# Kernel tuning notes

Hardware: AMD Instinct MI355X
Metric: run time of the kernel (lower is better)

The kernel has to match this reference:

```python
import jax, jax.numpy as jnp
import numpy as np

N = 8192
F_IN = 128
F_OUT = 128
NEG_SLOPE = 0.2


def setup_inputs() -> dict:
    key = jax.random.key(0)
    k_h, k_adj, k_W, k_a = jax.random.split(key, 4)
    h = jax.random.normal(k_h, (N, F_IN), dtype=jnp.float32)
    # binary adjacency mask as float (the module multiplies scores by adj)
    adj = (jax.random.uniform(k_adj, (N, N)) < 0.05).astype(jnp.float32)
    # nn.Linear(in, out, bias=False): weight shape [out, in]
    W = jax.random.normal(k_W, (F_OUT, F_IN), dtype=jnp.float32) / np.sqrt(F_IN)
    # nn.Linear(2*out, 1, bias=False): weight shape [1, 2*out]
    a = jax.random.normal(k_a, (1, 2 * F_OUT), dtype=jnp.float32) / np.sqrt(2 * F_OUT)
    return {"h": h, "adj": adj, "W": W, "a": a}


def reference(h, adj, W, a):
    # Wh: [N, F_out]
    Wh = h @ W.T
    f = Wh.shape[-1]
    # a([Wh_i ; Wh_j]) factored: e[i, j] = leaky_relu(Wh[i]@a1 + Wh[j]@a2)
    a1 = a[0, :f]  # [F_out]
    a2 = a[0, f:]  # [F_out]
    s_i = Wh @ a1  # [N]
    s_j = Wh @ a2  # [N]
    e = jax.nn.leaky_relu(s_i[:, None] + s_j[None, :], NEG_SLOPE)  # [N, N]
    # faithful to original: softmax over dim=1 of e * adj (multiplicative mask)
    attention = jax.nn.softmax(e * adj, axis=1)  # [N, N]
    return attention @ Wh  # [N, F_out]
```

## Files before the change

kernel.cpp:

```cpp
#include <hip/hip_runtime.h>

#define N_NODES 8192
#define FDIM 128
#define NEG_SLOPE 0.2f
#define SEG 512

__global__ __launch_bounds__(256) void wh_fused_kernel(
    const float* __restrict__ h, const float* __restrict__ W,
    float* __restrict__ Wh, float* __restrict__ S) {
  __shared__ float Wt[FDIM * 132];
  __shared__ float rows[32 * 132];
  const int t = threadIdx.x;
  const int base = blockIdx.x * 32;
  for (int it = 0; it < 64; ++it) {
    int idx = t + 256 * it;
    int o = idx >> 7, k = idx & 127;
    Wt[k * 132 + o] = W[idx];
  }
  for (int it = 0; it < 16; ++it) {
    int idx = t + 256 * it;
    int r = idx >> 7, col = idx & 127;
    rows[r * 132 + col] = h[(size_t)base * FDIM + idx];
  }
  __syncthreads();
  const int c4 = (t & 31) * 4;
  const int g = t >> 5;
  float acc[4][4];
#pragma unroll
  for (int rr = 0; rr < 4; ++rr)
#pragma unroll
    for (int cc = 0; cc < 4; ++cc) acc[rr][cc] = 0.f;
  for (int k = 0; k < FDIM; ++k) {
    float4 wv = *(const float4*)&Wt[k * 132 + c4];
    float rv[4];
#pragma unroll
    for (int rr = 0; rr < 4; ++rr) rv[rr] = rows[(4 * g + rr) * 132 + k];
#pragma unroll
    for (int rr = 0; rr < 4; ++rr) {
      acc[rr][0] += rv[rr] * wv.x;
      acc[rr][1] += rv[rr] * wv.y;
      acc[rr][2] += rv[rr] * wv.z;
      acc[rr][3] += rv[rr] * wv.w;
    }
  }
#pragma unroll
  for (int rr = 0; rr < 4; ++rr) {
    int r = base + 4 * g + rr;
    *(float4*)&Wh[(size_t)r * FDIM + c4] =
        make_float4(acc[rr][0], acc[rr][1], acc[rr][2], acc[rr][3]);
  }
  __syncthreads();
  float4 cs = make_float4(acc[0][0] + acc[1][0] + acc[2][0] + acc[3][0],
                          acc[0][1] + acc[1][1] + acc[2][1] + acc[3][1],
                          acc[0][2] + acc[1][2] + acc[2][2] + acc[3][2],
                          acc[0][3] + acc[1][3] + acc[2][3] + acc[3][3]);
  *(float4*)&rows[g * FDIM + c4] = cs;
  __syncthreads();
  if (t < FDIM) {
    float s = 0.f;
#pragma unroll
    for (int gg = 0; gg < 8; ++gg) s += rows[gg * FDIM + t];
    atomicAdd(&S[t], s);
  }
}

__global__ __launch_bounds__(256) void scores_kernel(
    const float* __restrict__ Wh, const float* __restrict__ a,
    float* __restrict__ s1, float* __restrict__ s2) {
  const int t = threadIdx.x;
  const int lane = t & 63;
  const int wave = t >> 6;
  const int row = blockIdx.x * 4 + wave;
  float v0 = Wh[(size_t)row * FDIM + lane];
  float v1 = Wh[(size_t)row * FDIM + 64 + lane];
  float d1 = v0 * a[lane] + v1 * a[64 + lane];
  float d2 = v0 * a[FDIM + lane] + v1 * a[FDIM + 64 + lane];
  for (int off = 32; off; off >>= 1) {
    d1 += __shfl_down(d1, off);
    d2 += __shfl_down(d2, off);
  }
  if (lane == 0) { s1[row] = d1; s2[row] = d2; }
}

__device__ __forceinline__ float4 ntload4(const float4* p) {
  typedef float f4v __attribute__((ext_vector_type(4)));
  f4v v = __builtin_nontemporal_load((const f4v*)p);
  return make_float4(v[0], v[1], v[2], v[3]);
}

__global__ __launch_bounds__(256, 4) void gat_row_kernel(
    const float* __restrict__ adj, const float* __restrict__ Wh,
    const float* __restrict__ s1, const float* __restrict__ s2,
    const float* __restrict__ S, float* __restrict__ out) {
  const int i = blockIdx.x;
  const int t = threadIdx.x;
  const int lane = t & 63;
  const int wave = t >> 6;
  __shared__ float2 pairs[4 * SEG];
  __shared__ int counts[4];
  __shared__ float red[4];
  __shared__ float red2[4];
  __shared__ float fpart[4][FDIM];

  const float s1i = s1[i];
  const float4* __restrict__ arow = (const float4*)(adj + (size_t)i * N_NODES);
  float2* __restrict__ mypairs = pairs + wave * SEG;
  const unsigned long long lmask = (1ull << lane) - 1ull;

  float4 av[8];
#pragma unroll
  for (int it = 0; it < 8; ++it) av[it] = ntload4(&arow[it * 256 + t]);
  asm volatile("" ::
      "v"(av[0].x), "v"(av[0].y), "v"(av[0].z), "v"(av[0].w),
      "v"(av[1].x), "v"(av[1].y), "v"(av[1].z), "v"(av[1].w),
      "v"(av[2].x), "v"(av[2].y), "v"(av[2].z), "v"(av[2].w),
      "v"(av[3].x), "v"(av[3].y), "v"(av[3].z), "v"(av[3].w),
      "v"(av[4].x), "v"(av[4].y), "v"(av[4].z), "v"(av[4].w),
      "v"(av[5].x), "v"(av[5].y), "v"(av[5].z), "v"(av[5].w),
      "v"(av[6].x), "v"(av[6].y), "v"(av[6].z), "v"(av[6].w),
      "v"(av[7].x), "v"(av[7].y), "v"(av[7].z), "v"(av[7].w));
  __builtin_amdgcn_sched_barrier(0);
  int cbase = 0;
#pragma unroll
  for (int it = 0; it < 8; ++it) {
    const int j4 = it * 256 + t;
    float v[4] = {av[it].x, av[it].y, av[it].z, av[it].w};
#pragma unroll
    for (int c = 0; c < 4; ++c) {
      bool pred = (v[c] != 0.f);
      unsigned long long b = __ballot(pred);
      if (pred) {
        int pos = cbase + (int)__popcll(b & lmask);
        if (pos < SEG) ((int*)&mypairs[pos])[1] = j4 * 4 + c;
      }
      cbase += (int)__popcll(b);
    }
  }
  const int mycnt = cbase < SEG ? cbase : SEG;
  if (lane == 0) counts[wave] = mycnt;

  float lmax = -1e30f;
  for (int k = lane; k < mycnt; k += 64) {
    int j = ((const int*)&mypairs[k])[1];
    float e = s1i + s2[j];
    e = e > 0.f ? e : NEG_SLOPE * e;
    mypairs[k].x = e;
    lmax = fmaxf(lmax, e);
  }
  for (int off = 32; off; off >>= 1) lmax = fmaxf(lmax, __shfl_down(lmax, off));
  if (lane == 0) red[wave] = lmax;
  __syncthreads();
  const int cnt = counts[0] + counts[1] + counts[2] + counts[3];
  float m = fmaxf(fmaxf(red[0], red[1]), fmaxf(red[2], red[3]));
  if (cnt < N_NODES) m = fmaxf(m, 0.f);
  const float em = __expf(-m);

  float lsum = 0.f;
  for (int k = lane; k < mycnt; k += 64) {
    float p = __expf(mypairs[k].x - m);
    mypairs[k].x = p;
    lsum += p;
  }
  for (int off = 32; off; off >>= 1) lsum += __shfl_down(lsum, off);
  if (lane == 0) red2[wave] = lsum;

  const int half = lane >> 5, lq = lane & 31;
  const float4* __restrict__ Wh4 = (const float4*)Wh;
  float ax = 0.f, ay = 0.f, az = 0.f, aw = 0.f;
  const int nit = (mycnt + 1) >> 1;
  int it = 0;
  for (; it + 3 < nit; it += 4) {
#pragma unroll
    for (int c = 0; c < 4; ++c) {
      int p = 2 * (it + c) + half;
      bool ok = p < mycnt;
      float2 pr = mypairs[ok ? p : 0];
      int j = ((const int*)&pr)[1];
      float4 v = Wh4[((size_t)j << 5) + lq];
      float w = ok ? pr.x - em : 0.f;
      ax += w * v.x; ay += w * v.y; az += w * v.z; aw += w * v.w;
    }
  }
  for (; it < nit; ++it) {
    int p = 2 * it + half;
    bool ok = p < mycnt;
    float2 pr = mypairs[ok ? p : 0];
    int j = ((const int*)&pr)[1];
    float4 v = Wh4[((size_t)j << 5) + lq];
    float w = ok ? pr.x - em : 0.f;
    ax += w * v.x; ay += w * v.y; az += w * v.z; aw += w * v.w;
  }
  ax += __shfl_down(ax, 32);
  ay += __shfl_down(ay, 32);
  az += __shfl_down(az, 32);
  aw += __shfl_down(aw, 32);
  if (lane < 32)
    *(float4*)&fpart[wave][4 * lq] = make_float4(ax, ay, az, aw);
  __syncthreads();
  if (t < FDIM) {
    float l = red2[0] + red2[1] + red2[2] + red2[3]
              + (float)(N_NODES - cnt) * em;
    float o = (fpart[0][t] + fpart[1][t] + fpart[2][t] + fpart[3][t]
               + em * S[t]) / l;
    out[(size_t)i * FDIM + t] = o;
  }
}

extern "C" void kernel_launch(void* const* d_in, const int* in_sizes, int n_in,
                              void* d_out, int out_size, void* d_ws, size_t ws_size,
                              hipStream_t stream) {
  const float* h   = (const float*)d_in[0];
  const float* adj = (const float*)d_in[1];
  const float* W   = (const float*)d_in[2];
  const float* a   = (const float*)d_in[3];
  float* out = (float*)d_out;
  float* Wh = (float*)d_ws;
  float* s1 = Wh + (size_t)N_NODES * FDIM;
  float* s2 = s1 + N_NODES;
  float* S  = s2 + N_NODES;

  hipMemsetAsync(S, 0, FDIM * sizeof(float), stream);
  hipLaunchKernelGGL(wh_fused_kernel, dim3(N_NODES / 32), dim3(256), 0, stream,
                     h, W, Wh, S);
  hipLaunchKernelGGL(scores_kernel, dim3(N_NODES / 4), dim3(256), 0, stream,
                     Wh, a, s1, s2);
  hipLaunchKernelGGL(gat_row_kernel, dim3(N_NODES), dim3(256), 0, stream,
                     adj, Wh, s1, s2, S, out);
}
```

Measured before the change: 430.1 us.

## Store Wh as bf16 for gather and fuse score computation into Wh kernel

Wh is now written in packed bf16 form, and the attention-weighted gather reads 8 bytes per lane instead of 16, which halves the gather traffic on the random neighbor rows. The s1/s2 score dot products are computed in the Wh GEMM kernel from fp32 accumulators, which removes the separate scores kernel and its reread of Wh. The cost is reduced precision in the aggregated output, since Wh values are rounded to bf16. The column sum S stays in fp32.

```diff
diff --git a/kernel.cpp b/kernel.cpp
--- a/kernel.cpp
+++ b/kernel.cpp
@@ -5,9 +5,17 @@
 #define NEG_SLOPE 0.2f
 #define SEG 512
 
+__device__ __forceinline__ unsigned int f2bf(float f) {
+  unsigned int u = __float_as_uint(f);
+  return (u + 0x7FFFu + ((u >> 16) & 1u)) >> 16;
+}
+
 __global__ __launch_bounds__(256) void wh_fused_kernel(
     const float* __restrict__ h, const float* __restrict__ W,
-    float* __restrict__ Wh, float* __restrict__ S) {
+    const float* __restrict__ a,
+    unsigned int* __restrict__ Whb,
+    float* __restrict__ s1, float* __restrict__ s2,
+    float* __restrict__ S) {
   __shared__ float Wt[FDIM * 132];
   __shared__ float rows[32 * 132];
   const int t = threadIdx.x;
@@ -46,8 +54,29 @@
 #pragma unroll
   for (int rr = 0; rr < 4; ++rr) {
     int r = base + 4 * g + rr;
-    *(float4*)&Wh[(size_t)r * FDIM + c4] =
-        make_float4(acc[rr][0], acc[rr][1], acc[rr][2], acc[rr][3]);
+    unsigned int p0 = f2bf(acc[rr][0]) | (f2bf(acc[rr][1]) << 16);
+    unsigned int p1 = f2bf(acc[rr][2]) | (f2bf(acc[rr][3]) << 16);
+    *(uint2*)&Whb[(size_t)r * 64 + (c4 >> 1)] = make_uint2(p0, p1);
+  }
+  {
+    float4 a1v = *(const float4*)&a[c4];
+    float4 a2v = *(const float4*)&a[FDIM + c4];
+#pragma unroll
+    for (int rr = 0; rr < 4; ++rr) {
+      float d1 = acc[rr][0] * a1v.x + acc[rr][1] * a1v.y +
+                 acc[rr][2] * a1v.z + acc[rr][3] * a1v.w;
+      float d2 = acc[rr][0] * a2v.x + acc[rr][1] * a2v.y +
+                 acc[rr][2] * a2v.z + acc[rr][3] * a2v.w;
+#pragma unroll
+      for (int off = 16; off; off >>= 1) {
+        d1 += __shfl_down(d1, off);
+        d2 += __shfl_down(d2, off);
+      }
+      if ((t & 31) == 0) {
+        s1[base + 4 * g + rr] = d1;
+        s2[base + 4 * g + rr] = d2;
+      }
+    }
   }
   __syncthreads();
   float4 cs = make_float4(acc[0][0] + acc[1][0] + acc[2][0] + acc[3][0],
@@ -64,24 +93,6 @@
   }
 }
 
-__global__ __launch_bounds__(256) void scores_kernel(
-    const float* __restrict__ Wh, const float* __restrict__ a,
-    float* __restrict__ s1, float* __restrict__ s2) {
-  const int t = threadIdx.x;
-  const int lane = t & 63;
-  const int wave = t >> 6;
-  const int row = blockIdx.x * 4 + wave;
-  float v0 = Wh[(size_t)row * FDIM + lane];
-  float v1 = Wh[(size_t)row * FDIM + 64 + lane];
-  float d1 = v0 * a[lane] + v1 * a[64 + lane];
-  float d2 = v0 * a[FDIM + lane] + v1 * a[FDIM + 64 + lane];
-  for (int off = 32; off; off >>= 1) {
-    d1 += __shfl_down(d1, off);
-    d2 += __shfl_down(d2, off);
-  }
-  if (lane == 0) { s1[row] = d1; s2[row] = d2; }
-}
-
 __device__ __forceinline__ float4 ntload4(const float4* p) {
   typedef float f4v __attribute__((ext_vector_type(4)));
   f4v v = __builtin_nontemporal_load((const f4v*)p);
@@ -89,7 +100,7 @@
 }
 
 __global__ __launch_bounds__(256, 4) void gat_row_kernel(
-    const float* __restrict__ adj, const float* __restrict__ Wh,
+    const float* __restrict__ adj, const unsigned int* __restrict__ Whb,
     const float* __restrict__ s1, const float* __restrict__ s2,
     const float* __restrict__ S, float* __restrict__ out) {
   const int i = blockIdx.x;
@@ -165,7 +176,7 @@
   if (lane == 0) red2[wave] = lsum;
 
   const int half = lane >> 5, lq = lane & 31;
-  const float4* __restrict__ Wh4 = (const float4*)Wh;
+  const uint2* __restrict__ Whb2 = (const uint2*)Whb;
   float ax = 0.f, ay = 0.f, az = 0.f, aw = 0.f;
   const int nit = (mycnt + 1) >> 1;
   int it = 0;
@@ -176,9 +187,12 @@
       bool ok = p < mycnt;
       float2 pr = mypairs[ok ? p : 0];
       int j = ((const int*)&pr)[1];
-      float4 v = Wh4[((size_t)j << 5) + lq];
+      uint2 d = Whb2[((size_t)j << 5) + lq];
       float w = ok ? pr.x - em : 0.f;
-      ax += w * v.x; ay += w * v.y; az += w * v.z; aw += w * v.w;
+      ax += w * __uint_as_float(d.x << 16);
+      ay += w * __uint_as_float(d.x & 0xffff0000u);
+      az += w * __uint_as_float(d.y << 16);
+      aw += w * __uint_as_float(d.y & 0xffff0000u);
     }
   }
   for (; it < nit; ++it) {
@@ -186,9 +200,12 @@
     bool ok = p < mycnt;
     float2 pr = mypairs[ok ? p : 0];
     int j = ((const int*)&pr)[1];
-    float4 v = Wh4[((size_t)j << 5) + lq];
+    uint2 d = Whb2[((size_t)j << 5) + lq];
     float w = ok ? pr.x - em : 0.f;
-    ax += w * v.x; ay += w * v.y; az += w * v.z; aw += w * v.w;
+    ax += w * __uint_as_float(d.x << 16);
+    ay += w * __uint_as_float(d.x & 0xffff0000u);
+    az += w * __uint_as_float(d.y << 16);
+    aw += w * __uint_as_float(d.y & 0xffff0000u);
   }
   ax += __shfl_down(ax, 32);
   ay += __shfl_down(ay, 32);
@@ -214,16 +231,14 @@
   const float* W   = (const float*)d_in[2];
   const float* a   = (const float*)d_in[3];
   float* out = (float*)d_out;
-  float* Wh = (float*)d_ws;
-  float* s1 = Wh + (size_t)N_NODES * FDIM;
+  unsigned int* Whb = (unsigned int*)d_ws;
+  float* s1 = (float*)(Whb + (size_t)N_NODES * 64);
   float* s2 = s1 + N_NODES;
   float* S  = s2 + N_NODES;
 
   hipMemsetAsync(S, 0, FDIM * sizeof(float), stream);
   hipLaunchKernelGGL(wh_fused_kernel, dim3(N_NODES / 32), dim3(256), 0, stream,
-                     h, W, Wh, S);
-  hipLaunchKernelGGL(scores_kernel, dim3(N_NODES / 4), dim3(256), 0, stream,
-                     Wh, a, s1, s2);
+                     h, W, a, Whb, s1, s2, S);
   hipLaunchKernelGGL(gat_row_kernel, dim3(N_NODES), dim3(256), 0, stream,
-                     adj, Wh, s1, s2, S, out);
-}
+                     adj, Whb, s1, s2, S, out);
+}
```

Measured after the change: 404.1 us. 1.06x faster.
